# Optimization experiments

Hardware: AMD Instinct MI355X
Metric: run time of the kernel (lower is better)

## Reference

```python
import jax, jax.numpy as jnp
import numpy as np

B, A, M, C = 8, 100000, 32, 80
IMG = 512.0


def setup_inputs():
    key = jax.random.key(0)
    k1, k2, k3, k4, k5, k6, k7, k8 = jax.random.split(key, 8)
    classifications = jax.random.uniform(k1, (B, A, C), jnp.float32)  # sigmoid-like probs
    regressions = jax.random.normal(k2, (B, A, 4), jnp.float32)
    # anchors: valid boxes (x1<x2, y1<y2) from centers + sizes
    ctr = jax.random.uniform(k3, (A, 2), jnp.float32, 0.0, IMG)
    wh = jax.random.uniform(k4, (A, 2), jnp.float32, 16.0, 256.0)
    anchors = jnp.concatenate([ctr - wh / 2, ctr + wh / 2], axis=-1)[None]  # [1,A,4]
    # annotations: [B,M,6] = x1,y1,x2,y2,class,aux_label (all valid, no -1 padding)
    gctr = jax.random.uniform(k5, (B, M, 2), jnp.float32, 32.0, IMG - 32.0)
    gwh = jax.random.uniform(k6, (B, M, 2), jnp.float32, 8.0, 128.0)
    boxes = jnp.concatenate([gctr - gwh / 2, gctr + gwh / 2], axis=-1)
    cls_ids = jax.random.randint(k7, (B, M, 1), 0, C).astype(jnp.float32)
    aux = jax.random.randint(k8, (B, M, 1), 0, 2).astype(jnp.float32)
    annotations = jnp.concatenate([boxes, cls_ids, aux], axis=-1)
    return {"classifications": classifications, "regressions": regressions,
            "anchors": anchors, "annotations": annotations}


def calc_iou(a, b):
    # a: [A,4] anchors, b: [M,4] gt boxes -> [A,M]
    area_a = ((a[:, 2] - a[:, 0]) * (a[:, 3] - a[:, 1]))[:, None]
    area_b = (b[:, 2] - b[:, 0]) * (b[:, 3] - b[:, 1])
    iw = jnp.minimum(a[:, 2:3], b[None, :, 2]) - jnp.maximum(a[:, 0:1], b[None, :, 0])
    ih = jnp.minimum(a[:, 3:4], b[None, :, 3]) - jnp.maximum(a[:, 1:2], b[None, :, 1])
    inter = jnp.clip(iw, 0.0) * jnp.clip(ih, 0.0)
    ua = jnp.clip(area_a + area_b[None, :] - inter, 1e-8)
    return inter / ua


def reference(classifications, regressions, anchors, annotations):
    alpha, gamma = 0.25, 2.0
    anchor = anchors[0]  # [A,4]
    aw = anchor[:, 2] - anchor[:, 0]
    ah = anchor[:, 3] - anchor[:, 1]
    acx = anchor[:, 0] + 0.5 * aw
    acy = anchor[:, 1] + 0.5 * ah
    std = jnp.array([0.1, 0.1, 0.2, 0.2], jnp.float32)

    def per_image(cls, reg, ann):
        valid = ann[:, 4] != -1.0  # padding mask (replaces dynamic filter)
        iou = calc_iou(anchor, ann[:, :4])  # [A,M]
        iou = jnp.where(valid[None, :], iou, -1.0)
        iou_max = iou.max(axis=1)
        iou_argmax = iou.argmax(axis=1)
        assigned = ann[iou_argmax]  # [A,6]
        cls = jnp.clip(cls, 1e-4, 1.0 - 1e-4)
        pos = iou_max >= 0.5
        num_pos = pos.sum().astype(jnp.float32)
        one_hot = jax.nn.one_hot(assigned[:, 4].astype(jnp.int32), cls.shape[1], dtype=cls.dtype)
        targets = jnp.where(pos[:, None], one_hot,
                            jnp.where((iou_max < 0.4)[:, None], 0.0, -1.0))
        alpha_factor = jnp.where(targets == 1.0, alpha, 1.0 - alpha)
        focal_w = alpha_factor * jnp.where(targets == 1.0, 1.0 - cls, cls) ** gamma
        bce = -(targets * jnp.log(cls) + (1.0 - targets) * jnp.log(1.0 - cls))
        cls_loss = jnp.where(targets != -1.0, focal_w * bce, 0.0)
        cls_loss = cls_loss.sum() / jnp.maximum(num_pos, 1.0)
        gw = assigned[:, 2] - assigned[:, 0]
        gh = assigned[:, 3] - assigned[:, 1]
        gcx = assigned[:, 0] + 0.5 * gw
        gcy = assigned[:, 1] + 0.5 * gh
        gw = jnp.clip(gw, 1.0)
        gh = jnp.clip(gh, 1.0)
        t = jnp.stack([(gcx - acx) / aw, (gcy - acy) / ah,
                       jnp.log(gw / aw), jnp.log(gh / ah)], axis=1) / std
        diff = jnp.abs(t - reg)
        rl = jnp.where(diff <= 1.0 / 9.0, 0.5 * 9.0 * diff ** 2, diff - 0.5 / 9.0)
        rl = jnp.where(pos[:, None], rl, 0.0)
        reg_loss = jnp.where(num_pos > 0,
                             rl.sum() / (4.0 * jnp.maximum(num_pos, 1.0)), 0.0)
        return cls_loss, reg_loss

    cl, rl = jax.vmap(per_image)(classifications, regressions, annotations)
    return cl.mean(keepdims=True), rl.mean(keepdims=True)
```

## Files before the change

### kernel.cpp

```cpp
#include <hip/hip_runtime.h>
#include <math.h>

#define B_IMG   8
#define A_ANCH  100000
#define M_ANN   32
#define C_CLS   80
#define TILE    256
#define NTHREADS 256
#define NWAVES  (NTHREADS/64)
#define V_PER_ANCH (C_CLS/4)
#define NBLK_X  ((A_ANCH + TILE - 1) / TILE)
#define PLANE   3200


__device__ __forceinline__ float focal4(float4 p4, int code, int c0) {
    const float m = (code != -1) ? 1.0f : 0.0f;
    float acc = 0.0f;
    const float pv[4] = {p4.x, p4.y, p4.z, p4.w};
    #pragma unroll
    for (int j = 0; j < 4; ++j) {
        const float p = fminf(fmaxf(pv[j], 1e-4f), 1.0f - 1e-4f);
        const bool t1 = (code == c0 + j);
        const float q = t1 ? (1.0f - p) : p;
        const float w = t1 ? 0.25f : 0.75f;
        acc = fmaf(m * w * q * q, -__logf(1.0f - q), acc);
    }
    return acc;
}

__global__ __launch_bounds__(NTHREADS, 1)
void focal_main(const float* __restrict__ cls,
                const float* __restrict__ regr,
                const float* __restrict__ anchors,
                const float* __restrict__ ann,
                float* __restrict__ part)
{
    __shared__ float s_ann[M_ANN][6];
    __shared__ float s_area[M_ANN];
    __shared__ int   s_code[TILE];
    __shared__ float s_red[3][NWAVES];

    const int b  = blockIdx.y;
    const int a0 = blockIdx.x * TILE;
    const int t  = threadIdx.x;

    if (t < M_ANN * 6) ((float*)s_ann)[t] = ann[(size_t)b * M_ANN * 6 + t];
    __syncthreads();
    if (t < M_ANN)
        s_area[t] = (s_ann[t][2] - s_ann[t][0]) * (s_ann[t][3] - s_ann[t][1]);
    __syncthreads();

    float reg_acc = 0.0f;
    float pos_cnt = 0.0f;

    const int a = a0 + t;
    if (a < A_ANCH) {
        const float4 ab = ((const float4*)anchors)[a];
        const float aw = ab.z - ab.x;
        const float ah = ab.w - ab.y;
        const float acx = ab.x + 0.5f * aw;
        const float acy = ab.y + 0.5f * ah;
        const float area_a = aw * ah;

        float best = -2.0f;
        int   bm   = 0;
        #pragma unroll 8
        for (int m = 0; m < M_ANN; ++m) {
            float iou;
            if (s_ann[m][4] == -1.0f) {
                iou = -1.0f;
            } else {
                float iw = fminf(ab.z, s_ann[m][2]) - fmaxf(ab.x, s_ann[m][0]);
                float ih = fminf(ab.w, s_ann[m][3]) - fmaxf(ab.y, s_ann[m][1]);
                float inter = fmaxf(iw, 0.0f) * fmaxf(ih, 0.0f);
                float ua = fmaxf(area_a + s_area[m] - inter, 1e-8f);
                iou = inter / ua;
            }
            if (iou > best) { best = iou; bm = m; }
        }

        const bool pos = (best >= 0.5f);
        int code;
        if (pos)                 code = (int)s_ann[bm][4];
        else if (best < 0.4f)    code = -2;
        else                     code = -1;
        s_code[t] = code;

        if (pos) {
            pos_cnt = 1.0f;
            const float gx1 = s_ann[bm][0], gy1 = s_ann[bm][1];
            const float gx2 = s_ann[bm][2], gy2 = s_ann[bm][3];
            float gw = gx2 - gx1, gh = gy2 - gy1;
            const float gcx = gx1 + 0.5f * gw;
            const float gcy = gy1 + 0.5f * gh;
            gw = fmaxf(gw, 1.0f); gh = fmaxf(gh, 1.0f);
            const float t0 = (gcx - acx) / aw * 10.0f;
            const float t1v = (gcy - acy) / ah * 10.0f;
            const float t2 = logf(gw / aw) * 5.0f;
            const float t3 = logf(gh / ah) * 5.0f;

            const float4 rg = ((const float4*)regr)[(size_t)b * A_ANCH + a];
            const float d0 = fabsf(t0  - rg.x);
            const float d1 = fabsf(t1v - rg.y);
            const float d2 = fabsf(t2  - rg.z);
            const float d3 = fabsf(t3  - rg.w);
            const float th = 1.0f / 9.0f;
            const float c_ = 0.5f / 9.0f;
            reg_acc += (d0 <= th) ? 4.5f * d0 * d0 : d0 - c_;
            reg_acc += (d1 <= th) ? 4.5f * d1 * d1 : d1 - c_;
            reg_acc += (d2 <= th) ? 4.5f * d2 * d2 : d2 - c_;
            reg_acc += (d3 <= th) ? 4.5f * d3 * d3 : d3 - c_;
        }
    } else {
        s_code[t] = -1;
    }
    __syncthreads();

    float cls_acc = 0.0f;
    const int n_anch = min(TILE, A_ANCH - a0);
    const float4* cbase = (const float4*)(cls + ((size_t)b * A_ANCH + a0) * C_CLS);

    if (n_anch == TILE) {
        float4 r[20];
        #pragma unroll
        for (int u = 0; u < 20; ++u)
            r[u] = cbase[t + u * NTHREADS];
        __builtin_amdgcn_sched_barrier(0);
        #pragma unroll
        for (int u = 0; u < 20; ++u) {
            const int v  = t + u * NTHREADS;
            const int al = v / V_PER_ANCH;
            const int c0 = (v - al * V_PER_ANCH) * 4;
            cls_acc += focal4(r[u], s_code[al], c0);
        }
    } else {
        const int nv = n_anch * V_PER_ANCH;
        for (int v = t; v < nv; v += NTHREADS) {
            const int al = v / V_PER_ANCH;
            const int c0 = (v - al * V_PER_ANCH) * 4;
            cls_acc += focal4(cbase[v], s_code[al], c0);
        }
    }

    #pragma unroll
    for (int off = 32; off > 0; off >>= 1) {
        cls_acc += __shfl_down(cls_acc, off, 64);
        reg_acc += __shfl_down(reg_acc, off, 64);
        pos_cnt += __shfl_down(pos_cnt, off, 64);
    }
    const int wave = t >> 6, lane = t & 63;
    if (lane == 0) {
        s_red[0][wave] = cls_acc;
        s_red[1][wave] = reg_acc;
        s_red[2][wave] = pos_cnt;
    }
    __syncthreads();
    if (t == 0) {
        float c = 0.f, r = 0.f, p = 0.f;
        #pragma unroll
        for (int w = 0; w < NWAVES; ++w) { c += s_red[0][w]; r += s_red[1][w]; p += s_red[2][w]; }
        const int idx = b * NBLK_X + blockIdx.x;
        part[idx]             = c;
        part[PLANE + idx]     = r;
        part[2 * PLANE + idx] = p;
    }
}

__global__ __launch_bounds__(256)
void focal_reduce(const float* __restrict__ part, float* __restrict__ out) {
    const int t = threadIdx.x;
    const int b = t >> 5;
    const int j = t & 31;
    float c = 0.f, r = 0.f, p = 0.f;
    for (int i = j; i < NBLK_X; i += 32) {
        const int idx = b * NBLK_X + i;
        c += part[idx];
        r += part[PLANE + idx];
        p += part[2 * PLANE + idx];
    }
    #pragma unroll
    for (int off = 16; off > 0; off >>= 1) {
        c += __shfl_down(c, off, 32);
        r += __shfl_down(r, off, 32);
        p += __shfl_down(p, off, 32);
    }
    __shared__ float s[B_IMG][3];
    if (j == 0) { s[b][0] = c; s[b][1] = r; s[b][2] = p; }
    __syncthreads();
    if (t == 0) {
        float cl = 0.f, rl = 0.f;
        #pragma unroll
        for (int bb = 0; bb < B_IMG; ++bb) {
            const float np  = s[bb][2];
            const float mnp = fmaxf(np, 1.0f);
            cl += s[bb][0] / mnp;
            rl += (np > 0.0f) ? s[bb][1] / (4.0f * mnp) : 0.0f;
        }
        out[0] = cl / (float)B_IMG;
        out[1] = rl / (float)B_IMG;
    }
}

extern "C" void kernel_launch(void* const* d_in, const int* in_sizes, int n_in,
                              void* d_out, int out_size, void* d_ws, size_t ws_size,
                              hipStream_t stream) {
    const float* cls     = (const float*)d_in[0];
    const float* regr    = (const float*)d_in[1];
    const float* anchors = (const float*)d_in[2];
    const float* ann     = (const float*)d_in[3];
    float* out  = (float*)d_out;
    float* part = (float*)d_ws;

    dim3 grid(NBLK_X, B_IMG);
    focal_main<<<grid, NTHREADS, 0, stream>>>(cls, regr, anchors, ann, part);
    focal_reduce<<<1, 256, 0, stream>>>(part, out);
}
```

Baseline: 378.7 us.

## Split anchor assignment and class-loss streaming into separate kernels

Anchor matching and regression loss move into their own kernel, which writes per-anchor class codes to workspace. A second grid-stride kernel with higher occupancy then streams the classification tensor, reads each anchor's code from global memory and accumulates focal loss. The aim is to decouple the latency-bound IoU loop from the bandwidth-bound stream and raise occupancy on the stream. In exchange it adds an extra launch, a global round trip for the codes, and drops the explicit 20-deep load batching.

```diff
diff --git a/kernel.cpp b/kernel.cpp
--- a/kernel.cpp
+++ b/kernel.cpp
@@ -5,13 +5,17 @@
 #define A_ANCH  100000
 #define M_ANN   32
 #define C_CLS   80
-#define TILE    256
 #define NTHREADS 256
 #define NWAVES  (NTHREADS/64)
 #define V_PER_ANCH (C_CLS/4)
-#define NBLK_X  ((A_ANCH + TILE - 1) / TILE)
-#define PLANE   3200
-
+#define AF4     (A_ANCH * V_PER_ANCH)
+#define NBLK_A  ((A_ANCH + NTHREADS - 1) / NTHREADS)
+#define NBLK_S  1024
+
+#define CLSPART_OFF 0
+#define REGPART_OFF 8192
+#define POSPART_OFF 12288
+#define CODES_OFF   16384
 
 __device__ __forceinline__ float focal4(float4 p4, int code, int c0) {
     const float m = (code != -1) ? 1.0f : 0.0f;
@@ -28,21 +32,20 @@
     return acc;
 }
 
-__global__ __launch_bounds__(NTHREADS, 1)
-void focal_main(const float* __restrict__ cls,
-                const float* __restrict__ regr,
-                const float* __restrict__ anchors,
-                const float* __restrict__ ann,
-                float* __restrict__ part)
+__global__ __launch_bounds__(NTHREADS)
+void focal_assign(const float* __restrict__ regr,
+                  const float* __restrict__ anchors,
+                  const float* __restrict__ ann,
+                  float* __restrict__ ws)
 {
     __shared__ float s_ann[M_ANN][6];
     __shared__ float s_area[M_ANN];
-    __shared__ int   s_code[TILE];
-    __shared__ float s_red[3][NWAVES];
+    __shared__ float s_red[2][NWAVES];
 
     const int b  = blockIdx.y;
-    const int a0 = blockIdx.x * TILE;
+    const int a0 = blockIdx.x * NTHREADS;
     const int t  = threadIdx.x;
+    int* __restrict__ codes = (int*)(ws + CODES_OFF);
 
     if (t < M_ANN * 6) ((float*)s_ann)[t] = ann[(size_t)b * M_ANN * 6 + t];
     __syncthreads();
@@ -84,7 +87,7 @@
         if (pos)                 code = (int)s_ann[bm][4];
         else if (best < 0.4f)    code = -2;
         else                     code = -1;
-        s_code[t] = code;
+        codes[(size_t)b * A_ANCH + a] = code;
 
         if (pos) {
             pos_cnt = 1.0f;
@@ -111,72 +114,68 @@
             reg_acc += (d2 <= th) ? 4.5f * d2 * d2 : d2 - c_;
             reg_acc += (d3 <= th) ? 4.5f * d3 * d3 : d3 - c_;
         }
-    } else {
-        s_code[t] = -1;
-    }
-    __syncthreads();
-
-    float cls_acc = 0.0f;
-    const int n_anch = min(TILE, A_ANCH - a0);
-    const float4* cbase = (const float4*)(cls + ((size_t)b * A_ANCH + a0) * C_CLS);
-
-    if (n_anch == TILE) {
-        float4 r[20];
-        #pragma unroll
-        for (int u = 0; u < 20; ++u)
-            r[u] = cbase[t + u * NTHREADS];
-        __builtin_amdgcn_sched_barrier(0);
-        #pragma unroll
-        for (int u = 0; u < 20; ++u) {
-            const int v  = t + u * NTHREADS;
-            const int al = v / V_PER_ANCH;
-            const int c0 = (v - al * V_PER_ANCH) * 4;
-            cls_acc += focal4(r[u], s_code[al], c0);
-        }
-    } else {
-        const int nv = n_anch * V_PER_ANCH;
-        for (int v = t; v < nv; v += NTHREADS) {
-            const int al = v / V_PER_ANCH;
-            const int c0 = (v - al * V_PER_ANCH) * 4;
-            cls_acc += focal4(cbase[v], s_code[al], c0);
-        }
     }
 
     #pragma unroll
     for (int off = 32; off > 0; off >>= 1) {
-        cls_acc += __shfl_down(cls_acc, off, 64);
         reg_acc += __shfl_down(reg_acc, off, 64);
         pos_cnt += __shfl_down(pos_cnt, off, 64);
     }
     const int wave = t >> 6, lane = t & 63;
-    if (lane == 0) {
-        s_red[0][wave] = cls_acc;
-        s_red[1][wave] = reg_acc;
-        s_red[2][wave] = pos_cnt;
-    }
+    if (lane == 0) { s_red[0][wave] = reg_acc; s_red[1][wave] = pos_cnt; }
     __syncthreads();
     if (t == 0) {
-        float c = 0.f, r = 0.f, p = 0.f;
+        float r = 0.f, p = 0.f;
         #pragma unroll
-        for (int w = 0; w < NWAVES; ++w) { c += s_red[0][w]; r += s_red[1][w]; p += s_red[2][w]; }
-        const int idx = b * NBLK_X + blockIdx.x;
-        part[idx]             = c;
-        part[PLANE + idx]     = r;
-        part[2 * PLANE + idx] = p;
+        for (int w = 0; w < NWAVES; ++w) { r += s_red[0][w]; p += s_red[1][w]; }
+        ws[REGPART_OFF + b * 512 + blockIdx.x] = r;
+        ws[POSPART_OFF + b * 512 + blockIdx.x] = p;
+    }
+}
+
+__global__ __launch_bounds__(NTHREADS, 8)
+void focal_stream(const float* __restrict__ cls,
+                  float* __restrict__ ws)
+{
+    const int b = blockIdx.y;
+    const int t = threadIdx.x;
+    const float4* __restrict__ cbase = (const float4*)cls + (size_t)b * AF4;
+    const int*    __restrict__ cb    = (const int*)(ws + CODES_OFF) + (size_t)b * A_ANCH;
+
+    float acc = 0.0f;
+    for (int v = blockIdx.x * NTHREADS + t; v < AF4; v += NBLK_S * NTHREADS) {
+        const int al = v / V_PER_ANCH;
+        const int c0 = (v - al * V_PER_ANCH) * 4;
+        const int code = cb[al];
+        acc += focal4(cbase[v], code, c0);
+    }
+
+    #pragma unroll
+    for (int off = 32; off > 0; off >>= 1)
+        acc += __shfl_down(acc, off, 64);
+    __shared__ float s_red[NWAVES];
+    const int wave = t >> 6, lane = t & 63;
+    if (lane == 0) s_red[wave] = acc;
+    __syncthreads();
+    if (t == 0) {
+        float c = 0.f;
+        #pragma unroll
+        for (int w = 0; w < NWAVES; ++w) c += s_red[w];
+        ws[CLSPART_OFF + b * NBLK_S + blockIdx.x] = c;
     }
 }
 
 __global__ __launch_bounds__(256)
-void focal_reduce(const float* __restrict__ part, float* __restrict__ out) {
+void focal_reduce(const float* __restrict__ ws, float* __restrict__ out) {
     const int t = threadIdx.x;
     const int b = t >> 5;
     const int j = t & 31;
     float c = 0.f, r = 0.f, p = 0.f;
-    for (int i = j; i < NBLK_X; i += 32) {
-        const int idx = b * NBLK_X + i;
-        c += part[idx];
-        r += part[PLANE + idx];
-        p += part[2 * PLANE + idx];
+    for (int i = j; i < NBLK_S; i += 32)
+        c += ws[CLSPART_OFF + b * NBLK_S + i];
+    for (int i = j; i < NBLK_A; i += 32) {
+        r += ws[REGPART_OFF + b * 512 + i];
+        p += ws[POSPART_OFF + b * 512 + i];
     }
     #pragma unroll
     for (int off = 16; off > 0; off >>= 1) {
@@ -208,10 +207,14 @@
     const float* regr    = (const float*)d_in[1];
     const float* anchors = (const float*)d_in[2];
     const float* ann     = (const float*)d_in[3];
-    float* out  = (float*)d_out;
-    float* part = (float*)d_ws;
-
-    dim3 grid(NBLK_X, B_IMG);
-    focal_main<<<grid, NTHREADS, 0, stream>>>(cls, regr, anchors, ann, part);
-    focal_reduce<<<1, 256, 0, stream>>>(part, out);
-}
+    float* out = (float*)d_out;
+    float* ws  = (float*)d_ws;
+
+    dim3 gA(NBLK_A, B_IMG);
+    focal_assign<<<gA, NTHREADS, 0, stream>>>(regr, anchors, ann, ws);
+
+    dim3 gS(NBLK_S, B_IMG);
+    focal_stream<<<gS, NTHREADS, 0, stream>>>(cls, ws);
+
+    focal_reduce<<<1, 256, 0, stream>>>(ws, out);
+}
```

New measurement: 388.9 us. 1.03x slower.
